# Kernel optimization log

Measured on AMD Instinct MI355X. Metric: run time of the kernel, lower is better.

The kernel has to match this reference:

```python
import jax, jax.numpy as jnp
import numpy as np

NUM_HEADS = 12
N_TOKENS = 1

def setup_inputs() -> dict:
    key = jax.random.key(0)
    ks = jax.random.split(key, 13)
    D = 768
    s = 0.02
    return {
        "x": jax.random.normal(ks[0], (64, 1025, D), jnp.float32),
        "qW": jax.random.normal(ks[1], (D, D), jnp.float32) * s,
        "qb": jax.random.normal(ks[2], (D,), jnp.float32) * s,
        "kW": jax.random.normal(ks[3], (D, D), jnp.float32) * s,
        "kb": jax.random.normal(ks[4], (D,), jnp.float32) * s,
        "vW": jax.random.normal(ks[5], (D, D), jnp.float32) * s,
        "vb": jax.random.normal(ks[6], (D,), jnp.float32) * s,
        "w1W": jax.random.normal(ks[7], (NUM_HEADS, NUM_HEADS), jnp.float32) * 0.1,
        "w1b": jax.random.normal(ks[8], (NUM_HEADS,), jnp.float32) * 0.1,
        "w2W": jax.random.normal(ks[9], (NUM_HEADS, NUM_HEADS), jnp.float32) * 0.1,
        "w2b": jax.random.normal(ks[10], (NUM_HEADS,), jnp.float32) * 0.1,
        "projW": jax.random.normal(ks[11], (D, D), jnp.float32) * s,
        "projb": jax.random.normal(ks[12], (D,), jnp.float32) * s,
    }

def reference(x, qW, qb, kW, kb, vW, vb, w1W, w1b, w2W, w2b, projW, projb):
    B, N, C = x.shape  # C == embed_dim == 768
    H = NUM_HEADS
    d = C // H
    scale = d ** -0.5
    cls = x[:, :N_TOKENS]  # [B, n, C]
    # torch Linear: y = x @ W.T + b
    q = (cls @ qW.T + qb).reshape(B, N_TOKENS, H, d).transpose(0, 2, 1, 3) * scale  # [B,H,n,d]
    k = (x @ kW.T + kb).reshape(B, N, H, d).transpose(0, 2, 1, 3)  # [B,H,N,d]
    v = (x @ vW.T + vb).reshape(B, N, H, d).transpose(0, 2, 1, 3)  # [B,H,N,d]
    attn = jnp.einsum('bhqd,bhkd->bhqk', q, k)  # [B,H,n,N]
    # talking-heads pre-softmax: linear over head dim, added residually
    attn = attn + jnp.einsum('bhqk,gh->bgqk', attn, w1W) + w1b[None, :, None, None]
    attn = jax.nn.softmax(attn, axis=-1)
    # talking-heads post-softmax
    attn = attn + jnp.einsum('bhqk,gh->bgqk', attn, w2W) + w2b[None, :, None, None]
    out = jnp.einsum('bhqk,bhkd->bhqd', attn, v)  # [B,H,n,d]
    out = out.transpose(0, 2, 1, 3).reshape(B, N_TOKENS, C)
    return out @ projW.T + projb
```

## Files before the change

kernel.cpp:

```cpp
#include <hip/hip_runtime.h>

#define B 64
#define N 1025
#define NPAD 1028
#define C 768
#define H 12
#define HD 64

__device__ __forceinline__ float wave_reduce_add(float v) {
    #pragma unroll
    for (int m = 1; m < 64; m <<= 1) v += __shfl_xor(v, m, 64);
    return v;
}

__global__ __launch_bounds__(256) void k_qproj(const float* __restrict__ x,
                                               const float* __restrict__ qW,
                                               const float* __restrict__ qb,
                                               float* __restrict__ qout) {
    __shared__ float cls[4 * C];
    int bt = blockIdx.x, ct = blockIdx.y, tid = threadIdx.x;
    for (int i = tid; i < 768; i += 256) {
        int bl = i / 192, c4 = i % 192;
        ((float4*)cls)[i] = ((const float4*)(x + (size_t)(bt * 4 + bl) * N * C))[c4];
    }
    __syncthreads();
    int w = tid >> 6, lane = tid & 63;
    int b = bt * 4 + w;
    const float* clsrow = &cls[w * C];
    for (int cl = 0; cl < 16; ++cl) {
        int c = ct * 16 + cl;
        const float4* wr = (const float4*)(qW + (size_t)c * C + lane * 12);
        const float4* xr = (const float4*)(clsrow + lane * 12);
        float acc = 0.f;
        #pragma unroll
        for (int s = 0; s < 3; ++s) {
            float4 a = wr[s], v = xr[s];
            acc += a.x * v.x + a.y * v.y + a.z * v.z + a.w * v.w;
        }
        acc = wave_reduce_add(acc);
        if (lane == 0) qout[b * C + c] = 0.125f * (acc + qb[c]);
    }
}

__global__ __launch_bounds__(256) void k_qk(const float* __restrict__ q,
                                            const float* __restrict__ kW,
                                            const float* __restrict__ kb,
                                            float* __restrict__ qk,
                                            float* __restrict__ qkb) {
    int bt = blockIdx.x, h = blockIdx.y, tid = threadIdx.x;
    if (tid < 192) {
        float4 acc[4] = {};
        #pragma unroll 4
        for (int i = 0; i < HD; ++i) {
            int row = h * HD + i;
            float4 kv = *(const float4*)(kW + (size_t)row * C + tid * 4);
            #pragma unroll
            for (int bl = 0; bl < 4; ++bl) {
                float qv = q[(bt * 4 + bl) * C + row];
                acc[bl].x += qv * kv.x; acc[bl].y += qv * kv.y;
                acc[bl].z += qv * kv.z; acc[bl].w += qv * kv.w;
            }
        }
        #pragma unroll
        for (int bl = 0; bl < 4; ++bl) {
            int b = bt * 4 + bl;
            *(float4*)(qk + ((size_t)b * H + h) * C + tid * 4) = acc[bl];
        }
    }
    int w = tid >> 6, lane = tid & 63;
    int b = bt * 4 + w;
    float v = q[b * C + h * HD + lane] * kb[h * HD + lane];
    v = wave_reduce_add(v);
    if (lane == 0) qkb[b * H + h] = v;
}

__global__ __launch_bounds__(256) void k_scores(const float* __restrict__ x,
                                                const float* __restrict__ qk,
                                                float* __restrict__ sc) {
    __shared__ float qs[12 * C];
    int tile = blockIdx.x, b = blockIdx.y, tid = threadIdx.x;
    const float4* qksrc = (const float4*)(qk + (size_t)b * H * C);
    for (int i = tid; i < 2304; i += 256) ((float4*)qs)[i] = qksrc[i];
    __syncthreads();
    int w = tid >> 6, lane = tid & 63;
    int c16 = lane & 15, r = lane >> 4;
    int rowbase = tile * 64 + w * 16 + r * 4;
    const float* xb = x + (size_t)b * N * C;
    float acc[4][12] = {};
    for (int cc = 0; cc < C; cc += 128) {
        int c0 = cc + c16 * 4, c1 = c0 + 64;
        float4 xv0[4], xv1[4];
        #pragma unroll
        for (int j = 0; j < 4; ++j) {
            int row = rowbase + j;
            const float* xr = xb + (size_t)row * C;
            xv0[j] = (row < N) ? *(const float4*)(xr + c0) : make_float4(0.f,0.f,0.f,0.f);
            xv1[j] = (row < N) ? *(const float4*)(xr + c1) : make_float4(0.f,0.f,0.f,0.f);
        }
        #pragma unroll
        for (int h = 0; h < 12; ++h) {
            float4 q0 = *(const float4*)(qs + h * C + c0);
            float4 q1 = *(const float4*)(qs + h * C + c1);
            #pragma unroll
            for (int j = 0; j < 4; ++j) {
                acc[j][h] += xv0[j].x * q0.x + xv0[j].y * q0.y +
                             xv0[j].z * q0.z + xv0[j].w * q0.w;
                acc[j][h] += xv1[j].x * q1.x + xv1[j].y * q1.y +
                             xv1[j].z * q1.z + xv1[j].w * q1.w;
            }
        }
    }
    #pragma unroll
    for (int j = 0; j < 4; ++j)
        #pragma unroll
        for (int h = 0; h < 12; ++h) {
            float v = acc[j][h];
            v += __shfl_xor(v, 1); v += __shfl_xor(v, 2);
            v += __shfl_xor(v, 4); v += __shfl_xor(v, 8);
            acc[j][h] = v;
        }
    if (c16 == 0) {
        #pragma unroll
        for (int j = 0; j < 4; ++j) {
            int row = rowbase + j;
            if (row < N) {
                #pragma unroll
                for (int h = 0; h < 12; ++h)
                    sc[((size_t)b * H + h) * NPAD + row] = acc[j][h];
            }
        }
    }
}

__global__ __launch_bounds__(256) void k_softmix(const float* __restrict__ sc,
                                                 const float* __restrict__ qkbias,
                                                 const float* __restrict__ w1W,
                                                 const float* __restrict__ w1b,
                                                 const float* __restrict__ w2W,
                                                 const float* __restrict__ w2b,
                                                 float* __restrict__ a2t,
                                                 float* __restrict__ s2) {
    __shared__ float sb[12 * NPAD];
    __shared__ float w1s[144], w1bs[12], w2s[144], w2bs[12];
    __shared__ float ms[12], invs[12], red[12];
    int b = blockIdx.x, tid = threadIdx.x;
    if (tid < 144) { w1s[tid] = w1W[tid]; w2s[tid] = w2W[tid]; }
    if (tid < 12)  { w1bs[tid] = w1b[tid]; w2bs[tid] = w2b[tid]; red[tid] = 0.f; }
    for (int i = tid; i < 12 * NPAD; i += 256) {
        int h = i / NPAD, n = i % NPAD;
        sb[i] = (n < N) ? sc[((size_t)b * H + h) * NPAD + n] + qkbias[b * H + h] : 0.f;
    }
    __syncthreads();
    for (int n = tid; n < N; n += 256) {
        float p[12], o[12];
        #pragma unroll
        for (int h = 0; h < 12; ++h) p[h] = sb[h * NPAD + n];
        #pragma unroll
        for (int g = 0; g < 12; ++g) {
            float a = p[g] + w1bs[g];
            #pragma unroll
            for (int h = 0; h < 12; ++h) a += w1s[g * 12 + h] * p[h];
            o[g] = a;
        }
        #pragma unroll
        for (int g = 0; g < 12; ++g) sb[g * NPAD + n] = o[g];
    }
    __syncthreads();
    int w = tid >> 6, lane = tid & 63;
    for (int g = w; g < 12; g += 4) {
        float m = -1e30f;
        for (int n = lane; n < N; n += 64) m = fmaxf(m, sb[g * NPAD + n]);
        #pragma unroll
        for (int k = 1; k < 64; k <<= 1) m = fmaxf(m, __shfl_xor(m, k, 64));
        float s = 0.f;
        for (int n = lane; n < N; n += 64) s += __expf(sb[g * NPAD + n] - m);
        s = wave_reduce_add(s);
        if (lane == 0) { ms[g] = m; invs[g] = 1.f / s; }
    }
    __syncthreads();
    float cs[12] = {};
    for (int n = tid; n < N; n += 256) {
        float p[12], o[12];
        #pragma unroll
        for (int h = 0; h < 12; ++h) p[h] = __expf(sb[h * NPAD + n] - ms[h]) * invs[h];
        #pragma unroll
        for (int g = 0; g < 12; ++g) {
            float a = p[g] + w2bs[g];
            #pragma unroll
            for (int h = 0; h < 12; ++h) a += w2s[g * 12 + h] * p[h];
            o[g] = a; cs[g] += a;
        }
        float* dst = a2t + ((size_t)b * N + n) * 12;
        #pragma unroll
        for (int g = 0; g < 12; ++g) dst[g] = o[g];
    }
    #pragma unroll
    for (int g = 0; g < 12; ++g) cs[g] = wave_reduce_add(cs[g]);
    if (lane == 0) {
        #pragma unroll
        for (int g = 0; g < 12; ++g) atomicAdd(&red[g], cs[g]);
    }
    __syncthreads();
    if (tid < 12) s2[b * H + tid] = red[tid];
}

#define FMA4(d, s, xv) { d.x += (s) * xv.x; d.y += (s) * xv.y; d.z += (s) * xv.z; d.w += (s) * xv.w; }
__global__ __launch_bounds__(192) void k_ysum(const float* __restrict__ x,
                                              const float* __restrict__ a2t,
                                              float* __restrict__ yp) {
    __shared__ float as_[129 * 12];
    int k = blockIdx.x, b = blockIdx.y, tid = threadIdx.x;
    int nlo = k * 128, nn = (k == 7) ? 129 : 128;
    const float4* ab = (const float4*)(a2t + ((size_t)b * N + nlo) * 12);
    for (int i = tid; i < nn * 3; i += 192) ((float4*)as_)[i] = ab[i];
    __syncthreads();
    const float* xb = x + ((size_t)b * N + nlo) * C + tid * 4;
    float4 acc[12] = {};
    int n = 0;
    for (; n + 4 <= nn; n += 4) {
        float4 xv[4];
        #pragma unroll
        for (int u = 0; u < 4; ++u)
            xv[u] = *(const float4*)(xb + (size_t)(n + u) * C);
        #pragma unroll
        for (int u = 0; u < 4; ++u) {
            const float4* ar = (const float4*)(as_ + (n + u) * 12);
            float4 a0 = ar[0], a1 = ar[1], a2 = ar[2];
            FMA4(acc[0], a0.x, xv[u]); FMA4(acc[1], a0.y, xv[u]); FMA4(acc[2], a0.z, xv[u]); FMA4(acc[3], a0.w, xv[u]);
            FMA4(acc[4], a1.x, xv[u]); FMA4(acc[5], a1.y, xv[u]); FMA4(acc[6], a1.z, xv[u]); FMA4(acc[7], a1.w, xv[u]);
            FMA4(acc[8], a2.x, xv[u]); FMA4(acc[9], a2.y, xv[u]); FMA4(acc[10], a2.z, xv[u]); FMA4(acc[11], a2.w, xv[u]);
        }
    }
    for (; n < nn; ++n) {
        float4 xv = *(const float4*)(xb + (size_t)n * C);
        const float4* ar = (const float4*)(as_ + n * 12);
        float4 a0 = ar[0], a1 = ar[1], a2 = ar[2];
        FMA4(acc[0], a0.x, xv); FMA4(acc[1], a0.y, xv); FMA4(acc[2], a0.z, xv); FMA4(acc[3], a0.w, xv);
        FMA4(acc[4], a1.x, xv); FMA4(acc[5], a1.y, xv); FMA4(acc[6], a1.z, xv); FMA4(acc[7], a1.w, xv);
        FMA4(acc[8], a2.x, xv); FMA4(acc[9], a2.y, xv); FMA4(acc[10], a2.z, xv); FMA4(acc[11], a2.w, xv);
    }
    #pragma unroll
    for (int h = 0; h < 12; ++h)
        *(float4*)(yp + (((size_t)k * B + b) * H + h) * C + tid * 4) = acc[h];
}

__global__ __launch_bounds__(256) void k_yred(const float* __restrict__ yp,
                                              float* __restrict__ y) {
    int i = blockIdx.x * 256 + threadIdx.x;
    const float4* src = (const float4*)yp;
    float4 s = make_float4(0.f, 0.f, 0.f, 0.f);
    #pragma unroll
    for (int k = 0; k < 8; ++k) {
        float4 v = src[(size_t)k * 147456 + i];
        s.x += v.x; s.y += v.y; s.z += v.z; s.w += v.w;
    }
    ((float4*)y)[i] = s;
}

__global__ __launch_bounds__(256) void k_zproj(const float* __restrict__ y,
                                               const float* __restrict__ vW,
                                               const float* __restrict__ vb,
                                               const float* __restrict__ s2,
                                               float* __restrict__ z) {
    __shared__ float ys[4 * C];
    int bt = blockIdx.x, ct = blockIdx.y, tid = threadIdx.x;
    int h = ct >> 2;
    for (int i = tid; i < 768; i += 256) {
        int bl = i / 192, c4 = i % 192;
        ((float4*)ys)[i] = ((const float4*)(y + (((size_t)(bt * 4 + bl)) * H + h) * C))[c4];
    }
    __syncthreads();
    int w = tid >> 6, lane = tid & 63;
    int b = bt * 4 + w;
    float sv = s2[b * H + h];
    const float* yrow = &ys[w * C];
    for (int cl = 0; cl < 16; ++cl) {
        int c = ct * 16 + cl;
        const float4* wr = (const float4*)(vW + (size_t)c * C + lane * 12);
        const float4* yr = (const float4*)(yrow + lane * 12);
        float acc = 0.f;
        #pragma unroll
        for (int s = 0; s < 3; ++s) {
            float4 a = wr[s], v = yr[s];
            acc += a.x * v.x + a.y * v.y + a.z * v.z + a.w * v.w;
        }
        acc = wave_reduce_add(acc);
        if (lane == 0) z[b * C + c] = acc + vb[c] * sv;
    }
}

__global__ __launch_bounds__(256) void k_out(const float* __restrict__ z,
                                             const float* __restrict__ pW,
                                             const float* __restrict__ pb,
                                             float* __restrict__ out) {
    __shared__ float zs[4 * C];
    int bt = blockIdx.x, ct = blockIdx.y, tid = threadIdx.x;
    for (int i = tid; i < 768; i += 256)
        ((float4*)zs)[i] = ((const float4*)(z + (size_t)bt * 4 * C))[i];
    __syncthreads();
    int w = tid >> 6, lane = tid & 63;
    int b = bt * 4 + w;
    for (int cl = 0; cl < 16; ++cl) {
        int c = ct * 16 + cl;
        const float4* wr = (const float4*)(pW + (size_t)c * C + lane * 12);
        const float4* zr = (const float4*)(zs + w * C + lane * 12);
        float acc = 0.f;
        #pragma unroll
        for (int s = 0; s < 3; ++s) {
            float4 a = wr[s], v = zr[s];
            acc += a.x * v.x + a.y * v.y + a.z * v.z + a.w * v.w;
        }
        acc = wave_reduce_add(acc);
        if (lane == 0) out[b * C + c] = acc + pb[c];
    }
}

extern "C" void kernel_launch(void* const* d_in, const int* in_sizes, int n_in,
                              void* d_out, int out_size, void* d_ws, size_t ws_size,
                              hipStream_t stream) {
    const float* x    = (const float*)d_in[0];
    const float* qW   = (const float*)d_in[1];
    const float* qb   = (const float*)d_in[2];
    const float* kW   = (const float*)d_in[3];
    const float* kb   = (const float*)d_in[4];
    const float* vW   = (const float*)d_in[5];
    const float* vb   = (const float*)d_in[6];
    const float* w1W  = (const float*)d_in[7];
    const float* w1b  = (const float*)d_in[8];
    const float* w2W  = (const float*)d_in[9];
    const float* w2b  = (const float*)d_in[10];
    const float* pW   = (const float*)d_in[11];
    const float* pb   = (const float*)d_in[12];
    float* out = (float*)d_out;

    float* ws   = (float*)d_ws;
    float* qk   = ws + 0;
    float* qkb  = ws + 589824;
    float* q    = ws + 590592;
    float* sc   = ws + 639744;
    float* y    = sc;
    float* a2t  = ws + 1429248;
    float* s2   = ws + 2216448;
    float* yp   = ws + 2217216;
    float* z    = ws + 6935808;

    k_qproj  <<<dim3(16, 48), 256, 0, stream>>>(x, qW, qb, q);
    k_qk     <<<dim3(16, 12), 256, 0, stream>>>(q, kW, kb, qk, qkb);
    k_scores <<<dim3(17, 64), 256, 0, stream>>>(x, qk, sc);
    k_softmix<<<64, 256, 0, stream>>>(sc, qkb, w1W, w1b, w2W, w2b, a2t, s2);
    k_ysum   <<<dim3(8, 64), 192, 0, stream>>>(x, a2t, yp);
    k_yred   <<<576, 256, 0, stream>>>(yp, y);
    k_zproj  <<<dim3(16, 48), 256, 0, stream>>>(y, vW, vb, s2, z);
    k_out    <<<dim3(16, 48), 256, 0, stream>>>(z, pW, pb, out);
}
```

Baseline: 466.6 us.

## Split softmax into parallel partial stats, fuse mix2 into ysum and yred into zproj

Replaces the 64-block softmix kernel with a k_mix1 kernel over 8x64 blocks that computes per-chunk max and sum-of-exp partials (online-softmax style). The post-softmax mix is recomputed inside k_ysum, so the a2t buffer round trip goes away, and the 8-way partial reduction is folded into k_zproj, which drops k_yred. The column sum s2 is replaced by a closed form (1 + N*w2b + row sum of w2W), using the fact that softmax rows sum to one. The goal is to remove the low-parallelism softmax kernel and one launch. The cost is that k_zproj now runs with only 192 blocks, each computing 64 outputs.

```diff
diff --git a/kernel.cpp b/kernel.cpp
--- a/kernel.cpp
+++ b/kernel.cpp
@@ -132,87 +132,111 @@
     }
 }
 
-__global__ __launch_bounds__(256) void k_softmix(const float* __restrict__ sc,
-                                                 const float* __restrict__ qkbias,
-                                                 const float* __restrict__ w1W,
-                                                 const float* __restrict__ w1b,
-                                                 const float* __restrict__ w2W,
-                                                 const float* __restrict__ w2b,
-                                                 float* __restrict__ a2t,
-                                                 float* __restrict__ s2) {
-    __shared__ float sb[12 * NPAD];
-    __shared__ float w1s[144], w1bs[12], w2s[144], w2bs[12];
-    __shared__ float ms[12], invs[12], red[12];
-    int b = blockIdx.x, tid = threadIdx.x;
-    if (tid < 144) { w1s[tid] = w1W[tid]; w2s[tid] = w2W[tid]; }
-    if (tid < 12)  { w1bs[tid] = w1b[tid]; w2bs[tid] = w2b[tid]; red[tid] = 0.f; }
-    for (int i = tid; i < 12 * NPAD; i += 256) {
-        int h = i / NPAD, n = i % NPAD;
-        sb[i] = (n < N) ? sc[((size_t)b * H + h) * NPAD + n] + qkbias[b * H + h] : 0.f;
-    }
-    __syncthreads();
-    for (int n = tid; n < N; n += 256) {
-        float p[12], o[12];
-        #pragma unroll
-        for (int h = 0; h < 12; ++h) p[h] = sb[h * NPAD + n];
+__global__ __launch_bounds__(256) void k_mix1(float* __restrict__ sc,
+                                              const float* __restrict__ qkbias,
+                                              const float* __restrict__ w1W,
+                                              const float* __restrict__ w1b,
+                                              float* __restrict__ mstat,
+                                              float* __restrict__ sstat) {
+    __shared__ float w1s[144], w1bs[12], qbs[12];
+    __shared__ float red[4][12];
+    __shared__ float mg[12];
+    int kk = blockIdx.x, b = blockIdx.y, tid = threadIdx.x;
+    int nn = (kk == 7) ? 129 : 128;
+    int n = kk * 128 + tid;
+    if (tid < 144) w1s[tid] = w1W[tid];
+    if (tid < 12)  { w1bs[tid] = w1b[tid]; qbs[tid] = qkbias[b * 12 + tid]; }
+    __syncthreads();
+    bool act = tid < nn;
+    float o[12];
+    if (act) {
+        float s_[12];
+        #pragma unroll
+        for (int h = 0; h < 12; ++h)
+            s_[h] = sc[((size_t)b * H + h) * NPAD + n] + qbs[h];
         #pragma unroll
         for (int g = 0; g < 12; ++g) {
-            float a = p[g] + w1bs[g];
+            float a = s_[g] + w1bs[g];
             #pragma unroll
-            for (int h = 0; h < 12; ++h) a += w1s[g * 12 + h] * p[h];
+            for (int h = 0; h < 12; ++h) a += w1s[g * 12 + h] * s_[h];
             o[g] = a;
         }
         #pragma unroll
-        for (int g = 0; g < 12; ++g) sb[g * NPAD + n] = o[g];
-    }
-    __syncthreads();
-    int w = tid >> 6, lane = tid & 63;
-    for (int g = w; g < 12; g += 4) {
-        float m = -1e30f;
-        for (int n = lane; n < N; n += 64) m = fmaxf(m, sb[g * NPAD + n]);
-        #pragma unroll
-        for (int k = 1; k < 64; k <<= 1) m = fmaxf(m, __shfl_xor(m, k, 64));
-        float s = 0.f;
-        for (int n = lane; n < N; n += 64) s += __expf(sb[g * NPAD + n] - m);
-        s = wave_reduce_add(s);
-        if (lane == 0) { ms[g] = m; invs[g] = 1.f / s; }
-    }
-    __syncthreads();
-    float cs[12] = {};
-    for (int n = tid; n < N; n += 256) {
-        float p[12], o[12];
-        #pragma unroll
-        for (int h = 0; h < 12; ++h) p[h] = __expf(sb[h * NPAD + n] - ms[h]) * invs[h];
+        for (int g = 0; g < 12; ++g)
+            sc[((size_t)b * H + g) * NPAD + n] = o[g];
+    } else {
+        #pragma unroll
+        for (int g = 0; g < 12; ++g) o[g] = -3e38f;
+    }
+    int w = tid >> 6, lane = tid & 63;
+    #pragma unroll
+    for (int g = 0; g < 12; ++g) {
+        float v = o[g];
+        #pragma unroll
+        for (int m = 1; m < 64; m <<= 1) v = fmaxf(v, __shfl_xor(v, m, 64));
+        if (lane == 0) red[w][g] = v;
+    }
+    __syncthreads();
+    if (tid < 12)
+        mg[tid] = fmaxf(fmaxf(red[0][tid], red[1][tid]),
+                        fmaxf(red[2][tid], red[3][tid]));
+    __syncthreads();
+    #pragma unroll
+    for (int g = 0; g < 12; ++g) {
+        float e = act ? __expf(o[g] - mg[g]) : 0.f;
+        e = wave_reduce_add(e);
+        if (lane == 0) red[w][g] = e;
+    }
+    __syncthreads();
+    if (tid < 12) {
+        mstat[((size_t)b * 8 + kk) * 12 + tid] = mg[tid];
+        sstat[((size_t)b * 8 + kk) * 12 + tid] =
+            red[0][tid] + red[1][tid] + red[2][tid] + red[3][tid];
+    }
+}
+
+#define FMA4(d, s, xv) { d.x += (s) * xv.x; d.y += (s) * xv.y; d.z += (s) * xv.z; d.w += (s) * xv.w; }
+__global__ __launch_bounds__(192) void k_ysum(const float* __restrict__ x,
+                                              const float* __restrict__ sc,
+                                              const float* __restrict__ mstat,
+                                              const float* __restrict__ sstat,
+                                              const float* __restrict__ w2W,
+                                              const float* __restrict__ w2b,
+                                              float* __restrict__ yp) {
+    __shared__ float as_[129 * 12];
+    __shared__ float w2s[144], w2bs[12], msh[12], ish[12];
+    int k = blockIdx.x, b = blockIdx.y, tid = threadIdx.x;
+    int nlo = k * 128, nn = (k == 7) ? 129 : 128;
+    if (tid < 144) w2s[tid] = w2W[tid];
+    if (tid < 12) {
+        w2bs[tid] = w2b[tid];
+        float m = -3e38f, mv[8];
+        #pragma unroll
+        for (int kk = 0; kk < 8; ++kk) {
+            mv[kk] = mstat[((size_t)b * 8 + kk) * 12 + tid];
+            m = fmaxf(m, mv[kk]);
+        }
+        float S = 0.f;
+        #pragma unroll
+        for (int kk = 0; kk < 8; ++kk)
+            S += sstat[((size_t)b * 8 + kk) * 12 + tid] * __expf(mv[kk] - m);
+        msh[tid] = m; ish[tid] = 1.f / S;
+    }
+    __syncthreads();
+    if (tid < nn) {
+        int n = nlo + tid;
+        float p[12];
+        #pragma unroll
+        for (int h = 0; h < 12; ++h)
+            p[h] = __expf(sc[((size_t)b * H + h) * NPAD + n] - msh[h]) * ish[h];
         #pragma unroll
         for (int g = 0; g < 12; ++g) {
             float a = p[g] + w2bs[g];
             #pragma unroll
             for (int h = 0; h < 12; ++h) a += w2s[g * 12 + h] * p[h];
-            o[g] = a; cs[g] += a;
-        }
-        float* dst = a2t + ((size_t)b * N + n) * 12;
-        #pragma unroll
-        for (int g = 0; g < 12; ++g) dst[g] = o[g];
-    }
-    #pragma unroll
-    for (int g = 0; g < 12; ++g) cs[g] = wave_reduce_add(cs[g]);
-    if (lane == 0) {
-        #pragma unroll
-        for (int g = 0; g < 12; ++g) atomicAdd(&red[g], cs[g]);
-    }
-    __syncthreads();
-    if (tid < 12) s2[b * H + tid] = red[tid];
-}
-
-#define FMA4(d, s, xv) { d.x += (s) * xv.x; d.y += (s) * xv.y; d.z += (s) * xv.z; d.w += (s) * xv.w; }
-__global__ __launch_bounds__(192) void k_ysum(const float* __restrict__ x,
-                                              const float* __restrict__ a2t,
-                                              float* __restrict__ yp) {
-    __shared__ float as_[129 * 12];
-    int k = blockIdx.x, b = blockIdx.y, tid = threadIdx.x;
-    int nlo = k * 128, nn = (k == 7) ? 129 : 128;
-    const float4* ab = (const float4*)(a2t + ((size_t)b * N + nlo) * 12);
-    for (int i = tid; i < nn * 3; i += 192) ((float4*)as_)[i] = ab[i];
+            as_[tid * 12 + g] = a;
+        }
+    }
     __syncthreads();
     const float* xb = x + ((size_t)b * N + nlo) * C + tid * 4;
     float4 acc[12] = {};
@@ -244,38 +268,34 @@
         *(float4*)(yp + (((size_t)k * B + b) * H + h) * C + tid * 4) = acc[h];
 }
 
-__global__ __launch_bounds__(256) void k_yred(const float* __restrict__ yp,
-                                              float* __restrict__ y) {
-    int i = blockIdx.x * 256 + threadIdx.x;
-    const float4* src = (const float4*)yp;
-    float4 s = make_float4(0.f, 0.f, 0.f, 0.f);
-    #pragma unroll
-    for (int k = 0; k < 8; ++k) {
-        float4 v = src[(size_t)k * 147456 + i];
-        s.x += v.x; s.y += v.y; s.z += v.z; s.w += v.w;
-    }
-    ((float4*)y)[i] = s;
-}
-
-__global__ __launch_bounds__(256) void k_zproj(const float* __restrict__ y,
+__global__ __launch_bounds__(256) void k_zproj(const float* __restrict__ yp,
                                                const float* __restrict__ vW,
                                                const float* __restrict__ vb,
-                                               const float* __restrict__ s2,
+                                               const float* __restrict__ w2W,
+                                               const float* __restrict__ w2b,
                                                float* __restrict__ z) {
     __shared__ float ys[4 * C];
-    int bt = blockIdx.x, ct = blockIdx.y, tid = threadIdx.x;
-    int h = ct >> 2;
+    int bt = blockIdx.x, h = blockIdx.y, tid = threadIdx.x;
     for (int i = tid; i < 768; i += 256) {
         int bl = i / 192, c4 = i % 192;
-        ((float4*)ys)[i] = ((const float4*)(y + (((size_t)(bt * 4 + bl)) * H + h) * C))[c4];
-    }
-    __syncthreads();
+        int b = bt * 4 + bl;
+        float4 s = make_float4(0.f, 0.f, 0.f, 0.f);
+        #pragma unroll
+        for (int k = 0; k < 8; ++k) {
+            float4 v = ((const float4*)(yp + (((size_t)k * B + b) * H + h) * C))[c4];
+            s.x += v.x; s.y += v.y; s.z += v.z; s.w += v.w;
+        }
+        ((float4*)ys)[i] = s;
+    }
+    __syncthreads();
+    float sv = 1.f + 1025.f * w2b[h];
+    #pragma unroll
+    for (int j = 0; j < 12; ++j) sv += w2W[h * 12 + j];
     int w = tid >> 6, lane = tid & 63;
     int b = bt * 4 + w;
-    float sv = s2[b * H + h];
     const float* yrow = &ys[w * C];
-    for (int cl = 0; cl < 16; ++cl) {
-        int c = ct * 16 + cl;
+    for (int cl = 0; cl < 64; ++cl) {
+        int c = h * 64 + cl;
         const float4* wr = (const float4*)(vW + (size_t)c * C + lane * 12);
         const float4* yr = (const float4*)(yrow + lane * 12);
         float acc = 0.f;
@@ -333,23 +353,21 @@
     const float* pb   = (const float*)d_in[12];
     float* out = (float*)d_out;
 
-    float* ws   = (float*)d_ws;
-    float* qk   = ws + 0;
-    float* qkb  = ws + 589824;
-    float* q    = ws + 590592;
-    float* sc   = ws + 639744;
-    float* y    = sc;
-    float* a2t  = ws + 1429248;
-    float* s2   = ws + 2216448;
-    float* yp   = ws + 2217216;
-    float* z    = ws + 6935808;
-
-    k_qproj  <<<dim3(16, 48), 256, 0, stream>>>(x, qW, qb, q);
-    k_qk     <<<dim3(16, 12), 256, 0, stream>>>(q, kW, kb, qk, qkb);
-    k_scores <<<dim3(17, 64), 256, 0, stream>>>(x, qk, sc);
-    k_softmix<<<64, 256, 0, stream>>>(sc, qkb, w1W, w1b, w2W, w2b, a2t, s2);
-    k_ysum   <<<dim3(8, 64), 192, 0, stream>>>(x, a2t, yp);
-    k_yred   <<<576, 256, 0, stream>>>(yp, y);
-    k_zproj  <<<dim3(16, 48), 256, 0, stream>>>(y, vW, vb, s2, z);
-    k_out    <<<dim3(16, 48), 256, 0, stream>>>(z, pW, pb, out);
-}
+    float* ws    = (float*)d_ws;
+    float* qk    = ws + 0;
+    float* qkb   = ws + 589824;
+    float* q     = ws + 590592;
+    float* sc    = ws + 639744;
+    float* yp    = ws + 1429248;
+    float* z     = ws + 6147840;
+    float* mstat = ws + 6196992;
+    float* sstat = ws + 6203136;
+
+    k_qproj <<<dim3(16, 48), 256, 0, stream>>>(x, qW, qb, q);
+    k_qk    <<<dim3(16, 12), 256, 0, stream>>>(q, kW, kb, qk, qkb);
+    k_scores<<<dim3(17, 64), 256, 0, stream>>>(x, qk, sc);
+    k_mix1  <<<dim3(8, 64), 256, 0, stream>>>(sc, qkb, w1W, w1b, mstat, sstat);
+    k_ysum  <<<dim3(8, 64), 192, 0, stream>>>(x, sc, mstat, sstat, w2W, w2b, yp);
+    k_zproj <<<dim3(16, 12), 256, 0, stream>>>(yp, vW, vb, w2W, w2b, z);
+    k_out   <<<dim3(16, 48), 256, 0, stream>>>(z, pW, pb, out);
+}
```

Result: no change. 458.9 us (-1.7%).
